# Optimization experiments

Measured on AMD Instinct MI355X. Metric: run time of the kernel, lower is better.

The kernel has to match this reference:

```python
import jax, jax.numpy as jnp
import numpy as np


def setup_inputs() -> dict:
    key = jax.random.key(0)
    k1, k2 = jax.random.split(key)
    B, H, W, D = 4096, 64, 64, 512
    inputs = jax.random.normal(k1, (B, D), dtype=jnp.float32)
    # keras 'random_uniform' initializer default range [-0.05, 0.05]
    weights_map = jax.random.uniform(k2, (H, W, D), dtype=jnp.float32,
                                     minval=-0.05, maxval=0.05)
    return {"inputs": inputs, "weights_map": weights_map}


def reference(inputs, weights_map):
    # inputs: (B, D); weights_map: (H, W, D)
    H, W, D = weights_map.shape
    flat_w = weights_map.reshape(-1, D)              # (N, D), N = H*W
    # avoids materializing the (B, N, D) difference tensor)
    x_sq = jnp.sum(inputs * inputs, axis=1, keepdims=True)    # (B, 1)
    w_sq = jnp.sum(flat_w * flat_w, axis=1)                   # (N,)
    sq_dist = x_sq - 2.0 * (inputs @ flat_w.T) + w_sq         # (B, N)
    sq_dist = jnp.maximum(sq_dist, 0.0)
    bmu_flat = jnp.argmin(sq_dist, axis=1)                    # (B,)
    bmu_y = (bmu_flat // W).astype(jnp.int32)
    bmu_x = (bmu_flat % W).astype(jnp.int32)
    bmu_indices = jnp.stack([bmu_y, bmu_x], axis=1)           # (B, 2)
    min_sq = jnp.take_along_axis(sq_dist, bmu_flat[:, None], axis=1)[:, 0]
    quantization_errors = jnp.sqrt(min_sq)                    # (B,)
    return bmu_indices, quantization_errors
```

## Files before the change

### kernel.cpp

```cpp
#include <hip/hip_runtime.h>

#define B_ROWS 4096
#define N_COLS 4096
#define DIM    512
#define LDK    1024

typedef __attribute__((ext_vector_type(8))) short short8;
typedef __attribute__((ext_vector_type(4))) float floatx4;

__device__ __forceinline__ unsigned short f2bf_rn(float f) {
    unsigned u = __float_as_uint(f);
    u += 0x7fffu + ((u >> 16) & 1u);
    return (unsigned short)(u >> 16);
}
__device__ __forceinline__ float bf2f(unsigned short h) {
    return __uint_as_float(((unsigned)h) << 16);
}

__device__ __forceinline__ unsigned long long pack_key(float v, int idx) {
    unsigned u = __float_as_uint(v);
    u = (u & 0x80000000u) ? ~u : (u | 0x80000000u);
    return ((unsigned long long)u << 32) | (unsigned)idx;
}

__device__ __forceinline__ void async16(const unsigned short* g, unsigned short* l) {
    __builtin_amdgcn_global_load_lds(
        (__attribute__((address_space(1))) void*)g,
        (__attribute__((address_space(3))) void*)l, 16, 0, 0);
}

__global__ __launch_bounds__(256) void som_convert(
    const float* __restrict__ X, const float* __restrict__ Wt,
    unsigned short* __restrict__ Xc, unsigned short* __restrict__ Wc,
    float* __restrict__ x_sq, float* __restrict__ w_sq,
    unsigned long long* __restrict__ packed)
{
    int wave = threadIdx.x >> 6, lane = threadIdx.x & 63;
    int grow = blockIdx.x * 4 + wave;
    bool isX = grow < B_ROWS;
    const float* src = isX ? (X + (size_t)grow * DIM)
                           : (Wt + (size_t)(grow - B_ROWS) * DIM);
    const float4* p4 = (const float4*)src;
    float4 a = p4[lane * 2], b = p4[lane * 2 + 1];
    float f[8] = {a.x, a.y, a.z, a.w, b.x, b.y, b.z, b.w};
    short8 hi, lo;
    float s = 0.f;
    #pragma unroll
    for (int t = 0; t < 8; ++t) {
        unsigned short h = f2bf_rn(f[t]);
        hi[t] = (short)h;
        lo[t] = (short)f2bf_rn(f[t] - bf2f(h));
        s = fmaf(f[t], f[t], s);
    }
    unsigned short* dst = (isX ? Xc + (size_t)grow * LDK
                               : Wc + (size_t)(grow - B_ROWS) * LDK) + lane * 8;
    *(short8*)(dst)       = hi;
    *(short8*)(dst + 512) = lo;
    #pragma unroll
    for (int off = 32; off >= 1; off >>= 1) s += __shfl_xor(s, off, 64);
    if (lane == 0) {
        if (isX) { x_sq[grow] = s; packed[grow] = ~0ull; }
        else     { w_sq[grow - B_ROWS] = s; }
    }
}

#define PH_TAIL(MF)                                            \
    __builtin_amdgcn_s_barrier();                              \
    asm volatile("s_waitcnt lgkmcnt(0)");                      \
    __builtin_amdgcn_s_setprio(1);                             \
    MF                                                         \
    __builtin_amdgcn_s_setprio(0);                             \
    __builtin_amdgcn_s_barrier();

#define MFMA16(AF, BF, I0)                                     \
    _Pragma("unroll")                                          \
    for (int i = 0; i < 4; ++i)                                \
        _Pragma("unroll")                                      \
        for (int j = 0; j < 4; ++j)                            \
            acc[(I0) + i][j] = __builtin_amdgcn_mfma_f32_16x16x32_bf16( \
                AF[i], BF[j], acc[(I0) + i][j], 0, 0, 0);

__global__ __launch_bounds__(512, 2) void som_dist_v4(
    const unsigned short* __restrict__ Xc, const unsigned short* __restrict__ Wc,
    const float* __restrict__ w_sq, unsigned long long* __restrict__ packed)
{
    __shared__ __align__(16) unsigned short L[2 * 64 * 512];
    const int tid  = threadIdx.x;
    const int wave = tid >> 6, lane = tid & 63;
    const int quad = lane >> 4, t16 = lane & 15;
    const int wr = wave >> 2, wc = wave & 3;

    const int bid = blockIdx.y * 16 + blockIdx.x;
    const int xcd = bid & 7, wix = bid >> 3;
    const int bm = (xcd >> 2) * 8 + (wix & 7);
    const int bn = (xcd & 3) * 4 + (wix >> 3);

    const int sg = wave & 3;
    const bool stB = (wave >= 4);
    const unsigned short* gsrc =
        (stB ? Wc + (size_t)bn * 256 * LDK : Xc + (size_t)bm * 256 * LDK)
        + (size_t)(sg * 64 + t16) * LDK + quad * 8;
    unsigned short* const lwav = &L[(stB ? 16384 : 0) + sg * 4096];

    const unsigned short* const pA = &L[wr * 8192 + lane * 8];
    const unsigned short* const pB = &L[16384 + wc * 4096 + lane * 8];

    floatx4 acc[8][4];
    #pragma unroll
    for (int i = 0; i < 8; ++i)
        #pragma unroll
        for (int j = 0; j < 4; ++j) acc[i][j] = (floatx4){0.f, 0.f, 0.f, 0.f};

    #pragma unroll
    for (int q = 0; q < 4; ++q) {
        async16(gsrc + q * 16 * LDK,       lwav + q * 1024);
        async16(gsrc + q * 16 * LDK + 512, lwav + q * 1024 + 512);
    }
    asm volatile("s_waitcnt vmcnt(0)");
    __builtin_amdgcn_s_barrier();
    __builtin_amdgcn_sched_barrier(0);

    #pragma unroll 1
    for (int kt = 0; kt < 16; ++kt) {
        const int cur = kt & 1;
        const unsigned short* pAc = pA + cur * 32768;
        const unsigned short* pBc = pB + cur * 32768;
        const bool st = (kt < 15);
        const unsigned short* gs = gsrc + (kt + 1) * 32;
        unsigned short* dst = lwav + (cur ^ 1) * 32768;

        short8 ah0[4], ah1[4], al0[4], al1[4], bh[4], bl[4];

        #pragma unroll
        for (int i = 0; i < 4; ++i) ah0[i] = *(const short8*)(pAc + i * 1024);
        #pragma unroll
        for (int j = 0; j < 4; ++j) bh[j]  = *(const short8*)(pBc + j * 1024);
        if (st) {
            async16(gs,                 dst);
            async16(gs + 512,           dst + 512);
            async16(gs + 16 * LDK,      dst + 1024);
            async16(gs + 16 * LDK + 512, dst + 1536);
        }
        PH_TAIL(MFMA16(ah0, bh, 0))

        #pragma unroll
        for (int j = 0; j < 4; ++j) bl[j] = *(const short8*)(pBc + j * 1024 + 512);
        if (st) {
            async16(gs + 32 * LDK,       dst + 2048);
            async16(gs + 32 * LDK + 512, dst + 2560);
            async16(gs + 48 * LDK,       dst + 3072);
            async16(gs + 48 * LDK + 512, dst + 3584);
        }
        PH_TAIL(MFMA16(ah0, bl, 0))

        #pragma unroll
        for (int i = 0; i < 4; ++i) al0[i] = *(const short8*)(pAc + i * 1024 + 512);
        PH_TAIL(MFMA16(al0, bh, 0))

        #pragma unroll
        for (int i = 0; i < 4; ++i) ah1[i] = *(const short8*)(pAc + (4 + i) * 1024);
        PH_TAIL(MFMA16(ah1, bh, 4))

        #pragma unroll
        for (int i = 0; i < 4; ++i) al1[i] = *(const short8*)(pAc + (4 + i) * 1024 + 512);
        PH_TAIL(MFMA16(ah1, bl, 4))

        asm volatile("s_waitcnt lgkmcnt(0)");
        __builtin_amdgcn_s_setprio(1);
        MFMA16(al1, bh, 4)
        __builtin_amdgcn_s_setprio(0);

        asm volatile("s_waitcnt vmcnt(0)");
        __builtin_amdgcn_s_barrier();
        __builtin_amdgcn_sched_barrier(0);
    }

    const int col0 = bn * 256 + wc * 64 + t16;
    float wq[4];
    #pragma unroll
    for (int j = 0; j < 4; ++j) wq[j] = w_sq[col0 + j * 16];
    const int row_base = bm * 256 + wr * 128 + quad * 4;
    #pragma unroll
    for (int i = 0; i < 8; ++i) {
        #pragma unroll
        for (int r = 0; r < 4; ++r) {
            unsigned long long best = ~0ull;
            #pragma unroll
            for (int j = 0; j < 4; ++j) {
                float val = fmaf(-2.f, acc[i][j][r], wq[j]);
                unsigned long long key = pack_key(val, col0 + j * 16);
                best = (key < best) ? key : best;
            }
            #pragma unroll
            for (int m = 1; m <= 8; m <<= 1) {
                unsigned long long o = __shfl_xor(best, m, 64);
                best = (o < best) ? o : best;
            }
            if (t16 == 0)
                atomicMin(&packed[row_base + i * 16 + r], best);
        }
    }
}

__global__ __launch_bounds__(256) void som_finalize(
    const unsigned long long* __restrict__ packed,
    const float* __restrict__ x_sq, float* __restrict__ out)
{
    int b = blockIdx.x * 256 + threadIdx.x;
    unsigned long long p = packed[b];
    unsigned idx = (unsigned)(p & 0xffffffffull);
    unsigned key = (unsigned)(p >> 32);
    unsigned u = (key & 0x80000000u) ? (key & 0x7fffffffu) : ~key;
    float val = __uint_as_float(u);
    float sq = fmaxf(x_sq[b] + val, 0.f);
    out[2 * b]     = (float)(idx >> 6);
    out[2 * b + 1] = (float)(idx & 63);
    out[2 * B_ROWS + b] = sqrtf(sq);
}

extern "C" void kernel_launch(void* const* d_in, const int* in_sizes, int n_in,
                              void* d_out, int out_size, void* d_ws, size_t ws_size,
                              hipStream_t stream) {
    const float* X  = (const float*)d_in[0];
    const float* Wt = (const float*)d_in[1];
    float* out = (float*)d_out;

    unsigned long long* packed = (unsigned long long*)d_ws;
    float* x_sq = (float*)((char*)d_ws + (32 << 10));
    float* w_sq = (float*)((char*)d_ws + (48 << 10));
    unsigned short* Xc = (unsigned short*)((char*)d_ws + (64 << 10));
    unsigned short* Wc = (unsigned short*)((char*)d_ws + (64 << 10) + ((size_t)B_ROWS * LDK * 2));

    som_convert<<<dim3((B_ROWS + N_COLS) / 4), dim3(256), 0, stream>>>(
        X, Wt, Xc, Wc, x_sq, w_sq, packed);
    som_dist_v4<<<dim3(N_COLS / 256, B_ROWS / 256), dim3(512), 0, stream>>>(
        Xc, Wc, w_sq, packed);
    som_finalize<<<dim3(B_ROWS / 256), dim3(256), 0, stream>>>(packed, x_sq, out);
}
```

Baseline: 124.4 us.

## Split async tile loads by hi/lo halves and use partial vmcnt waits

```diff
diff --git a/kernel.cpp b/kernel.cpp
--- a/kernel.cpp
+++ b/kernel.cpp
@@ -64,13 +64,12 @@
     }
 }
 
-#define PH_TAIL(MF)                                            \
+#define PH_CORE(MF)                                            \
     __builtin_amdgcn_s_barrier();                              \
     asm volatile("s_waitcnt lgkmcnt(0)");                      \
     __builtin_amdgcn_s_setprio(1);                             \
     MF                                                         \
-    __builtin_amdgcn_s_setprio(0);                             \
-    __builtin_amdgcn_s_barrier();
+    __builtin_amdgcn_s_setprio(0);
 
 #define MFMA16(AF, BF, I0)                                     \
     _Pragma("unroll")                                          \
@@ -80,7 +79,7 @@
             acc[(I0) + i][j] = __builtin_amdgcn_mfma_f32_16x16x32_bf16( \
                 AF[i], BF[j], acc[(I0) + i][j], 0, 0, 0);
 
-__global__ __launch_bounds__(512, 2) void som_dist_v4(
+__global__ __launch_bounds__(512, 2) void som_dist_v5(
     const unsigned short* __restrict__ Xc, const unsigned short* __restrict__ Wc,
     const float* __restrict__ w_sq, unsigned long long* __restrict__ packed)
 {
@@ -112,13 +111,12 @@
         for (int j = 0; j < 4; ++j) acc[i][j] = (floatx4){0.f, 0.f, 0.f, 0.f};
 
     #pragma unroll
-    for (int q = 0; q < 4; ++q) {
-        async16(gsrc + q * 16 * LDK,       lwav + q * 1024);
-        async16(gsrc + q * 16 * LDK + 512, lwav + q * 1024 + 512);
-    }
-    asm volatile("s_waitcnt vmcnt(0)");
+    for (int q = 0; q < 4; ++q) async16(gsrc + q * 16 * LDK, lwav + q * 1024);
+    #pragma unroll
+    for (int q = 0; q < 4; ++q) async16(gsrc + q * 16 * LDK + 512, lwav + q * 1024 + 512);
+    asm volatile("s_waitcnt vmcnt(4)");
+    __builtin_amdgcn_sched_barrier(0);
     __builtin_amdgcn_s_barrier();
-    __builtin_amdgcn_sched_barrier(0);
 
     #pragma unroll 1
     for (int kt = 0; kt < 16; ++kt) {
@@ -136,43 +134,55 @@
         #pragma unroll
         for (int j = 0; j < 4; ++j) bh[j]  = *(const short8*)(pBc + j * 1024);
         if (st) {
-            async16(gs,                 dst);
-            async16(gs + 512,           dst + 512);
-            async16(gs + 16 * LDK,      dst + 1024);
+            async16(gs,            dst);
+            async16(gs + 16 * LDK, dst + 1024);
+        }
+        PH_CORE(MFMA16(ah0, bh, 0))
+        if (kt == 15) asm volatile("s_waitcnt vmcnt(0)");
+        else          asm volatile("s_waitcnt vmcnt(2)");
+        __builtin_amdgcn_sched_barrier(0);
+        __builtin_amdgcn_s_barrier();
+
+        #pragma unroll
+        for (int j = 0; j < 4; ++j) bl[j] = *(const short8*)(pBc + j * 1024 + 512);
+        if (st) {
+            async16(gs + 32 * LDK, dst + 2048);
+            async16(gs + 48 * LDK, dst + 3072);
+        }
+        PH_CORE(MFMA16(ah0, bl, 0))
+        __builtin_amdgcn_s_barrier();
+
+        #pragma unroll
+        for (int i = 0; i < 4; ++i) al0[i] = *(const short8*)(pAc + i * 1024 + 512);
+        if (st) {
+            async16(gs + 512,            dst + 512);
             async16(gs + 16 * LDK + 512, dst + 1536);
         }
-        PH_TAIL(MFMA16(ah0, bh, 0))
-
-        #pragma unroll
-        for (int j = 0; j < 4; ++j) bl[j] = *(const short8*)(pBc + j * 1024 + 512);
-        if (st) {
-            async16(gs + 32 * LDK,       dst + 2048);
+        PH_CORE(MFMA16(al0, bh, 0))
+        __builtin_amdgcn_s_barrier();
+
+        #pragma unroll
+        for (int i = 0; i < 4; ++i) ah1[i] = *(const short8*)(pAc + (4 + i) * 1024);
+        if (st) {
             async16(gs + 32 * LDK + 512, dst + 2560);
-            async16(gs + 48 * LDK,       dst + 3072);
             async16(gs + 48 * LDK + 512, dst + 3584);
         }
-        PH_TAIL(MFMA16(ah0, bl, 0))
-
-        #pragma unroll
-        for (int i = 0; i < 4; ++i) al0[i] = *(const short8*)(pAc + i * 1024 + 512);
-        PH_TAIL(MFMA16(al0, bh, 0))
-
-        #pragma unroll
-        for (int i = 0; i < 4; ++i) ah1[i] = *(const short8*)(pAc + (4 + i) * 1024);
-        PH_TAIL(MFMA16(ah1, bh, 4))
+        PH_CORE(MFMA16(ah1, bh, 4))
+        __builtin_amdgcn_s_barrier();
 
         #pragma unroll
         for (int i = 0; i < 4; ++i) al1[i] = *(const short8*)(pAc + (4 + i) * 1024 + 512);
-        PH_TAIL(MFMA16(ah1, bl, 4))
+        PH_CORE(MFMA16(ah1, bl, 4))
+        __builtin_amdgcn_s_barrier();
 
         asm volatile("s_waitcnt lgkmcnt(0)");
         __builtin_amdgcn_s_setprio(1);
         MFMA16(al1, bh, 4)
         __builtin_amdgcn_s_setprio(0);
 
-        asm volatile("s_waitcnt vmcnt(0)");
-        __builtin_amdgcn_s_barrier();
+        asm volatile("s_waitcnt vmcnt(4)");
         __builtin_amdgcn_sched_barrier(0);
+        __builtin_amdgcn_s_barrier();
     }
 
     const int col0 = bn * 256 + wc * 64 + t16;
@@ -233,7 +243,7 @@
 
     som_convert<<<dim3((B_ROWS + N_COLS) / 4), dim3(256), 0, stream>>>(
         X, Wt, Xc, Wc, x_sq, w_sq, packed);
-    som_dist_v4<<<dim3(N_COLS / 256, B_ROWS / 256), dim3(512), 0, stream>>>(
+    som_dist_v5<<<dim3(N_COLS / 256, B_ROWS / 256), dim3(512), 0, stream>>>(
         Xc, Wc, w_sq, packed);
     som_finalize<<<dim3(B_ROWS / 256), dim3(256), 0, stream>>>(packed, x_sq, out);
 }
```

Measured after the change: 116.7 us. -6.2%, faster.
